# Optimization experiments

Measured on AMD Instinct MI355X. Metric: run time of the kernel, lower is better.

## Reference

```python
import jax, jax.numpy as jnp
import numpy as np

N = 20000          # num nodes
E = 250000         # num edges
B = 128            # num graphs in batch
Fin = 512
Fqk = 512
Fv = 512
H = 8              # nheads


def setup_inputs() -> dict:
    key = jax.random.key(0)
    k1, k2, k3, k4 = jax.random.split(key, 4)
    x = jax.random.normal(k1, (N, Fin), dtype=jnp.float32)
    batch = jnp.sort(jax.random.randint(k2, (N,), 0, B)).astype(jnp.int32)
    ei = jax.random.randint(k3, (2, E), 0, N).astype(jnp.int32)
    # proj weight of Linear(Fin, 2*Fqk+Fv, bias=False); stored as (Fin, Ftot)
    W = (jax.random.normal(k4, (Fin, 2 * Fqk + Fv), dtype=jnp.float32)
         / np.sqrt(Fin).astype(np.float32))
    return {"x": x, "batch": batch, "ei": ei, "W": W}


def reference(x, batch, ei, W):
    src, dest = ei[0], ei[1]
    n = x.shape[0]
    Fh = Fqk // H            # head dim for q/k
    Fhv = Fv // H            # head dim for v
    scaling = float(Fh) ** (-0.5)

    qkv = x @ W                                    # (N, 2*Fqk+Fv)
    q, k, v = jnp.split(qkv, [Fqk, 2 * Fqk], axis=-1)
    q = (q * scaling).reshape(n, H, Fh)
    k = k.reshape(n, H, Fh)
    v = v.reshape(n, H, Fhv)

    # edge-wise gathers
    qs = q[src]                                    # (E, H, Fh)
    ks = k[dest]                                   # (E, H, Fh)
    vs = v[dest]                                   # (E, H, Fhv)

    # per-edge, per-head attention scores
    aw = jnp.einsum('ehf,ehf->eh', qs, ks)         # (E, H)

    # segment softmax over edges sharing the same src node (stable)
    m = jax.ops.segment_max(aw, src, num_segments=n)       # (N, H)
    e = jnp.exp(aw - m[src])                                # (E, H)
    denom = jax.ops.segment_sum(e, src, num_segments=n)     # (N, H)
    alpha = e / denom[src]                                   # (E, H)

    # scatter-weighted aggregation of values back to src nodes
    out = jax.ops.segment_sum(alpha[:, :, None] * vs, src, num_segments=n)  # (N, H, Fhv)
    return out.reshape(n, Fv)
```

## Files before the change

### kernel.cpp

```cpp
#include <hip/hip_runtime.h>
#include <cstdint>

typedef float f32x4 __attribute__((ext_vector_type(4)));
typedef __bf16 bf16x8 __attribute__((ext_vector_type(8)));

__device__ __forceinline__ unsigned short f2b(float f) {
  unsigned int u = __float_as_uint(f);
  u = (u + 0x7fffu + ((u >> 16) & 1u)) >> 16;
  return (unsigned short)u;
}

__device__ __forceinline__ void unpack8(uint4 u, float* f) {
  f[0] = __uint_as_float((u.x & 0xffffu) << 16);
  f[1] = __uint_as_float(u.x & 0xffff0000u);
  f[2] = __uint_as_float((u.y & 0xffffu) << 16);
  f[3] = __uint_as_float(u.y & 0xffff0000u);
  f[4] = __uint_as_float((u.z & 0xffffu) << 16);
  f[5] = __uint_as_float(u.z & 0xffff0000u);
  f[6] = __uint_as_float((u.w & 0xffffu) << 16);
  f[7] = __uint_as_float(u.w & 0xffff0000u);
}

__device__ __forceinline__ void async_copy16(const void* g, void* l) {
  __builtin_amdgcn_global_load_lds(
      (const __attribute__((address_space(1))) void*)g,
      (__attribute__((address_space(3))) void*)l, 16, 0, 0);
}

__global__ __launch_bounds__(256) void prep_kernel(
    const float* __restrict__ W, unsigned short* __restrict__ Wt, int NT) {
  __shared__ float tile[32][33];
  int b = blockIdx.x, t = threadIdx.x;
  int tilesPerRow = NT / 32;
  int n0 = (b % tilesPerRow) * 32, k0 = (b / tilesPerRow) * 32;
  int r = t >> 5, c = t & 31;
#pragma unroll
  for (int ph = 0; ph < 4; ++ph)
    tile[r + 8 * ph][c] = W[(size_t)(k0 + r + 8 * ph) * NT + n0 + c];
  __syncthreads();
#pragma unroll
  for (int ph = 0; ph < 4; ++ph) {
    int rr = r + 8 * ph;
    int nn = n0 + rr;
    float s = (nn < 512) ? 0.125f : 1.0f;
    Wt[(size_t)nn * 512 + k0 + c] = f2b(tile[c][rr] * s);
  }
}

__global__ __launch_bounds__(1024, 4) void gemm256_kernel(
    const float* __restrict__ X, const unsigned short* __restrict__ Bt,
    unsigned short* __restrict__ C, int K, int NT, int NPAN, int nrows,
    int GEMMB, const int* __restrict__ src, const int* __restrict__ dst,
    int* __restrict__ deg, int* __restrict__ edst, int E) {
  __shared__ __align__(16) unsigned short SM[49152];

  int bx = blockIdx.x, tid = threadIdx.x;

  if (bx >= GEMMB) {
    int e = (bx - GEMMB) * 1024 + tid;
    if (e < E) {
      int s = src[e], d = dst[e];
      int j = atomicAdd(&deg[s], 1);
      if (j < 64) edst[(size_t)s * 64 + j] = d;
    }
    return;
  }

  int nwg = GEMMB;
  int q8 = nwg >> 3, r8 = nwg & 7;
  int xcd = bx & 7, idx = bx >> 3;
  int wgid = (xcd < r8 ? xcd * (q8 + 1) : r8 * (q8 + 1) + (xcd - r8) * q8) + idx;
  int mtile = wgid / NPAN, npanel = wgid % NPAN;
  int m0 = mtile * 256, n0 = npanel * 256;

  int wave = tid >> 6, lane = tid & 63;
  int wm = wave >> 2, wn = wave & 3;
  int hi = lane >> 4, l15 = lane & 15;

  int srow = (tid >> 6) * 16 + l15;
  int scol = ((tid >> 4) & 3) * 8;
  bool inb = (m0 + srow) < nrows;
  const float* pX = X + (size_t)(m0 + srow) * K + scol;
  const unsigned short* pB = Bt + (size_t)(n0 + srow) * K + scol;

  auto loadA = [&](int t, float4& f0, float4& f1) {
    if (inb) {
      f0 = *(const float4*)(pX + t * 32);
      f1 = *(const float4*)(pX + t * 32 + 4);
    } else {
      f0 = make_float4(0.f, 0.f, 0.f, 0.f);
      f1 = make_float4(0.f, 0.f, 0.f, 0.f);
    }
  };
  auto cvtWriteA = [&](const float4& f0, const float4& f1, int slot) {
    uint4 w;
    w.x = (unsigned)f2b(f0.x) | ((unsigned)f2b(f0.y) << 16);
    w.y = (unsigned)f2b(f0.z) | ((unsigned)f2b(f0.w) << 16);
    w.z = (unsigned)f2b(f1.x) | ((unsigned)f2b(f1.y) << 16);
    w.w = (unsigned)f2b(f1.z) | ((unsigned)f2b(f1.w) << 16);
    *(uint4*)(SM + slot * 8192 + tid * 8) = w;
  };

  async_copy16(pB, SM + 24576 + tid * 8);
  async_copy16(pB + 32, SM + 24576 + 8192 + tid * 8);
  __builtin_amdgcn_sched_barrier(0);
  float4 f00, f01, nf0, nf1;
  loadA(0, f00, f01);
  loadA(1, nf0, nf1);
  __builtin_amdgcn_sched_barrier(0);
  cvtWriteA(f00, f01, 0);
  asm volatile("s_waitcnt lgkmcnt(0)" ::: "memory");
  __builtin_amdgcn_s_barrier();
  __builtin_amdgcn_sched_barrier(0);

  f32x4 acc[4][4] = {};
  int aoff = wm * 2048 + lane * 8;
  int boff = 24576 + wn * 2048 + lane * 8;

#pragma unroll
  for (int t = 0; t < 16; ++t) {
    int sb = (t % 3) * 8192;
    bf16x8 av[4], bv[4];
    const unsigned short* a_ = SM + sb + aoff;
    const unsigned short* b_ = SM + sb + boff;
#pragma unroll
    for (int i = 0; i < 4; ++i) av[i] = *(const bf16x8*)(a_ + i * 512);
#pragma unroll
    for (int j = 0; j < 4; ++j) bv[j] = *(const bf16x8*)(b_ + j * 512);
    if (t + 2 < 16) {
      int s2 = ((t + 2) % 3) * 8192;
      async_copy16(pB + (t + 2) * 32, SM + 24576 + s2 + tid * 8);
    }
    if (t + 1 < 16) cvtWriteA(nf0, nf1, (t + 1) % 3);
    if (t + 2 < 16) loadA(t + 2, nf0, nf1);
    __builtin_amdgcn_s_setprio(1);
#pragma unroll
    for (int i = 0; i < 4; ++i)
#pragma unroll
      for (int j = 0; j < 4; ++j)
        acc[i][j] = __builtin_amdgcn_mfma_f32_16x16x32_bf16(av[i], bv[j], acc[i][j], 0, 0, 0);
    __builtin_amdgcn_s_setprio(0);
    if (t + 2 < 16) {
      asm volatile("s_waitcnt vmcnt(2)" ::: "memory");
    } else {
      asm volatile("s_waitcnt vmcnt(0)" ::: "memory");
    }
    asm volatile("s_waitcnt lgkmcnt(0)" ::: "memory");
    __builtin_amdgcn_sched_barrier(0);
    __builtin_amdgcn_s_barrier();
    __builtin_amdgcn_sched_barrier(0);
  }

  __syncthreads();
  unsigned short* cs = SM + wave * 640;
  unsigned short* gC = C + (size_t)(m0 + wm * 64) * NT + n0 + wn * 64;
  int erow = lane >> 2, echunk = (lane & 3) * 8;
#pragma unroll
  for (int i = 0; i < 4; ++i)
#pragma unroll
    for (int p = 0; p < 2; ++p) {
#pragma unroll
      for (int jj = 0; jj < 2; ++jj)
#pragma unroll
        for (int q = 0; q < 4; ++q)
          cs[(hi * 4 + q) * 40 + jj * 16 + l15] = f2b(acc[i][2 * p + jj][q]);
      uint4 val = *(const uint4*)&cs[erow * 40 + echunk];
      *(uint4*)&gC[(size_t)(i * 16 + erow) * NT + p * 32 + echunk] = val;
    }
}

__global__ __launch_bounds__(256) void attn_kernel(
    const unsigned short* __restrict__ qkv, const int* __restrict__ deg,
    const int* __restrict__ edst, float* __restrict__ out, int n, int nwtot) {
  int gw = blockIdx.x * 4 + (threadIdx.x >> 6);
  int lane = threadIdx.x & 63;

  for (int node = gw; node < n; node += nwtot) {
    float q[8];
    unpack8(*(const uint4*)(qkv + (size_t)node * 1536 + lane * 8), q);

    float acc[8] = {0.f, 0.f, 0.f, 0.f, 0.f, 0.f, 0.f, 0.f};
    float l = 0.f;
    int dn = deg[node];
    if (dn > 64) dn = 64;
    int beg = node * 64, end = beg + dn;

    int i = beg;
    for (; i + 4 <= end; i += 4) {
      int d0 = edst[i], d1 = edst[i + 1], d2 = edst[i + 2], d3 = edst[i + 3];
      const uint4* p0 = (const uint4*)(qkv + (size_t)d0 * 1536 + 512 + lane * 8);
      const uint4* p1 = (const uint4*)(qkv + (size_t)d1 * 1536 + 512 + lane * 8);
      const uint4* p2 = (const uint4*)(qkv + (size_t)d2 * 1536 + 512 + lane * 8);
      const uint4* p3 = (const uint4*)(qkv + (size_t)d3 * 1536 + 512 + lane * 8);
      uint4 kr0 = p0[0], vr0 = p0[64];
      uint4 kr1 = p1[0], vr1 = p1[64];
      uint4 kr2 = p2[0], vr2 = p2[64];
      uint4 kr3 = p3[0], vr3 = p3[64];
#pragma unroll
      for (int u = 0; u < 4; ++u) {
        uint4 kv = (u == 0) ? kr0 : (u == 1) ? kr1 : (u == 2) ? kr2 : kr3;
        uint4 vv = (u == 0) ? vr0 : (u == 1) ? vr1 : (u == 2) ? vr2 : vr3;
        float kf[8], vf[8];
        unpack8(kv, kf);
        unpack8(vv, vf);
        float part = 0.f;
#pragma unroll
        for (int j = 0; j < 8; ++j) part = fmaf(q[j], kf[j], part);
        part += __shfl_xor(part, 1);
        part += __shfl_xor(part, 2);
        part += __shfl_xor(part, 4);
        float p = __expf(part);
        l += p;
#pragma unroll
        for (int j = 0; j < 8; ++j) acc[j] = fmaf(p, vf[j], acc[j]);
      }
    }
    for (; i < end; ++i) {
      int d = edst[i];
      const uint4* pp = (const uint4*)(qkv + (size_t)d * 1536 + 512 + lane * 8);
      uint4 kv = pp[0], vv = pp[64];
      float kf[8], vf[8];
      unpack8(kv, kf);
      unpack8(vv, vf);
      float part = 0.f;
#pragma unroll
      for (int j = 0; j < 8; ++j) part = fmaf(q[j], kf[j], part);
      part += __shfl_xor(part, 1);
      part += __shfl_xor(part, 2);
      part += __shfl_xor(part, 4);
      float p = __expf(part);
      l += p;
#pragma unroll
      for (int j = 0; j < 8; ++j) acc[j] = fmaf(p, vf[j], acc[j]);
    }

    float inv = (l > 0.f) ? 1.f / l : 0.f;
    float4 o0, o1;
    o0.x = acc[0] * inv; o0.y = acc[1] * inv; o0.z = acc[2] * inv; o0.w = acc[3] * inv;
    o1.x = acc[4] * inv; o1.y = acc[5] * inv; o1.z = acc[6] * inv; o1.w = acc[7] * inv;
    float4* op = (float4*)(out + (size_t)node * 512 + lane * 8);
    op[0] = o0;
    op[1] = o1;
  }
}

extern "C" void kernel_launch(void* const* d_in, const int* in_sizes, int n_in,
                              void* d_out, int out_size, void* d_ws, size_t ws_size,
                              hipStream_t stream) {
  const float* x = (const float*)d_in[0];
  const int* ei = (const int*)d_in[2];
  const float* W = (const float*)d_in[3];
  float* out = (float*)d_out;

  const int N = in_sizes[1];
  const int E = in_sizes[2] / 2;
  const int Fin = in_sizes[0] / N;
  const int FT = in_sizes[3] / Fin;
  const int MPAD = ((N + 255) / 256) * 256;

  const int* src = ei;
  const int* dst = ei + E;

  char* ws = (char*)d_ws;
  size_t off = 0;
  auto alloc = [&](size_t bytes) {
    void* p = ws + off;
    off = (off + bytes + 255) & ~(size_t)255;
    return p;
  };
  unsigned short* Wt  = (unsigned short*)alloc((size_t)FT * Fin * 2);
  unsigned short* qkv = (unsigned short*)alloc((size_t)MPAD * FT * 2);
  int* deg  = (int*)alloc((size_t)N * 4);
  int* edst = (int*)alloc((size_t)N * 64 * 4);

  hipMemsetAsync(deg, 0, (size_t)N * 4, stream);

  int nbConvw = (FT / 32) * (Fin / 32);
  prep_kernel<<<nbConvw, 256, 0, stream>>>(W, Wt, FT);

  int NPAN = FT / 256;
  int MTILES = MPAD / 256;
  int GEMMB = MTILES * NPAN;
  int nbBucket = (E + 1023) / 1024;
  gemm256_kernel<<<GEMMB + nbBucket, 1024, 0, stream>>>(
      x, Wt, qkv, Fin, FT, NPAN, N, GEMMB, src, dst, deg, edst, E);

  int attnBlocks = 1024;
  attn_kernel<<<attnBlocks, 256, 0, stream>>>(qkv, deg, edst, out, N,
                                              attnBlocks * 4);
}
```

Baseline: 147.8 us.

## Deepen GEMM K-loop pipeline to four LDS stages with longer prefetch distance

The GEMM main loop moves from a 3-slot LDS ring with 2-step-ahead prefetch to a 4-slot ring. W tiles are prefetched 3 steps ahead and X tiles are loaded into registers 4 steps ahead, with two alternating register sets. The aim is to hide more global-memory latency behind the MFMA work, and the final iteration's barrier is skipped. In exchange, LDS per block grows from 96KB to 128KB, which may limit how many blocks fit per CU, and more registers stay live. The hand-tuned vmcnt counts must match the order in which loads are issued.

```diff
diff --git a/kernel.cpp b/kernel.cpp
--- a/kernel.cpp
+++ b/kernel.cpp
@@ -52,7 +52,7 @@
     unsigned short* __restrict__ C, int K, int NT, int NPAN, int nrows,
     int GEMMB, const int* __restrict__ src, const int* __restrict__ dst,
     int* __restrict__ deg, int* __restrict__ edst, int E) {
-  __shared__ __align__(16) unsigned short SM[49152];
+  __shared__ __align__(16) unsigned short SM[65536];
 
   int bx = blockIdx.x, tid = threadIdx.x;
 
@@ -101,38 +101,46 @@
     *(uint4*)(SM + slot * 8192 + tid * 8) = w;
   };
 
-  async_copy16(pB, SM + 24576 + tid * 8);
-  async_copy16(pB + 32, SM + 24576 + 8192 + tid * 8);
-  __builtin_amdgcn_sched_barrier(0);
-  float4 f00, f01, nf0, nf1;
-  loadA(0, f00, f01);
-  loadA(1, nf0, nf1);
-  __builtin_amdgcn_sched_barrier(0);
-  cvtWriteA(f00, f01, 0);
+  float4 t0a, t0b, t1a, t1b;
+  float4 s0a, s0b, s1a, s1b;
+  loadA(0, t0a, t0b);
+  loadA(1, t1a, t1b);
+  loadA(2, s0a, s0b);
+  loadA(3, s1a, s1b);
+  async_copy16(pB, SM + 32768 + tid * 8);
+  async_copy16(pB + 32, SM + 32768 + 8192 + tid * 8);
+  async_copy16(pB + 64, SM + 32768 + 16384 + tid * 8);
+  cvtWriteA(t0a, t0b, 0);
+  cvtWriteA(t1a, t1b, 1);
+  asm volatile("s_waitcnt vmcnt(1)" ::: "memory");
   asm volatile("s_waitcnt lgkmcnt(0)" ::: "memory");
   __builtin_amdgcn_s_barrier();
   __builtin_amdgcn_sched_barrier(0);
 
   f32x4 acc[4][4] = {};
   int aoff = wm * 2048 + lane * 8;
-  int boff = 24576 + wn * 2048 + lane * 8;
+  int boff = 32768 + wn * 2048 + lane * 8;
 
 #pragma unroll
   for (int t = 0; t < 16; ++t) {
-    int sb = (t % 3) * 8192;
+    int sa = (t & 3) * 8192;
     bf16x8 av[4], bv[4];
-    const unsigned short* a_ = SM + sb + aoff;
-    const unsigned short* b_ = SM + sb + boff;
+    const unsigned short* a_ = SM + sa + aoff;
+    const unsigned short* b_ = SM + sa + boff;
 #pragma unroll
     for (int i = 0; i < 4; ++i) av[i] = *(const bf16x8*)(a_ + i * 512);
 #pragma unroll
     for (int j = 0; j < 4; ++j) bv[j] = *(const bf16x8*)(b_ + j * 512);
-    if (t + 2 < 16) {
-      int s2 = ((t + 2) % 3) * 8192;
-      async_copy16(pB + (t + 2) * 32, SM + 24576 + s2 + tid * 8);
-    }
-    if (t + 1 < 16) cvtWriteA(nf0, nf1, (t + 1) % 3);
-    if (t + 2 < 16) loadA(t + 2, nf0, nf1);
+    if (t <= 13) {
+      if ((t & 1) == 0) cvtWriteA(s0a, s0b, (t + 2) & 3);
+      else              cvtWriteA(s1a, s1b, (t + 2) & 3);
+    }
+    if (t <= 11) {
+      if ((t & 1) == 0) loadA(t + 4, s0a, s0b);
+      else              loadA(t + 4, s1a, s1b);
+    }
+    if (t <= 12)
+      async_copy16(pB + (t + 3) * 32, SM + 32768 + ((t + 3) & 3) * 8192 + tid * 8);
     __builtin_amdgcn_s_setprio(1);
 #pragma unroll
     for (int i = 0; i < 4; ++i)
@@ -140,15 +148,21 @@
       for (int j = 0; j < 4; ++j)
         acc[i][j] = __builtin_amdgcn_mfma_f32_16x16x32_bf16(av[i], bv[j], acc[i][j], 0, 0, 0);
     __builtin_amdgcn_s_setprio(0);
-    if (t + 2 < 16) {
-      asm volatile("s_waitcnt vmcnt(2)" ::: "memory");
-    } else {
+    if (t <= 11) {
+      asm volatile("s_waitcnt vmcnt(6)" ::: "memory");
+    } else if (t == 12) {
+      asm volatile("s_waitcnt vmcnt(4)" ::: "memory");
+    } else if (t == 13) {
+      asm volatile("s_waitcnt vmcnt(1)" ::: "memory");
+    } else if (t == 14) {
       asm volatile("s_waitcnt vmcnt(0)" ::: "memory");
     }
-    asm volatile("s_waitcnt lgkmcnt(0)" ::: "memory");
-    __builtin_amdgcn_sched_barrier(0);
-    __builtin_amdgcn_s_barrier();
-    __builtin_amdgcn_sched_barrier(0);
+    if (t < 15) {
+      asm volatile("s_waitcnt lgkmcnt(0)" ::: "memory");
+      __builtin_amdgcn_sched_barrier(0);
+      __builtin_amdgcn_s_barrier();
+      __builtin_amdgcn_sched_barrier(0);
+    }
   }
 
   __syncthreads();
```

After: 195.5 us. 1.32x slower.
